# Kernel optimization log

Measured on AMD Instinct MI355X. Metric: run time of the kernel, lower is better.

Reference implementation:

```python
import jax, jax.numpy as jnp
import numpy as np

D, P = 50, 2          # feature dim and max polynomial order (module defaults)
N = 32768             # batch size

def _indexset(d, p):
    # faithful numpy port of indexset(): all multi-indices of total order exactly p
    if d == 1:
        return np.full((1, 1), p, dtype=np.int64)
    blocks = []
    for i in range(p + 1):
        sub = _indexset(d - 1, p - i)
        blocks.append(np.concatenate([np.full((sub.shape[0], 1), i, np.int64), sub], axis=1))
    return np.concatenate(blocks, axis=0)

def _normal_basis(p):
    # faithful numpy port of NormalBasis(): (physicists') Hermite recurrence coefficients
    B = np.zeros((p + 1, p + 1), np.float32)
    B[0, 0] = 1.0
    if p >= 1:
        B[1, 1] = 2.0
    for i in range(1, p):
        B[i + 1, 1:i + 2] = 2.0 * B[i, :i + 1]
        B[i + 1, :i] -= 2.0 * i * B[i - 1, :i]
    return B

def setup_inputs() -> dict:
    key = jax.random.key(0)
    k1, k2 = jax.random.split(key)
    x = jax.random.normal(k1, (N, D), dtype=jnp.float32)
    mean = jax.random.normal(k2, (D,), dtype=jnp.float32)
    var = jnp.ones((D,), dtype=jnp.float32)  # divisor; ones keeps values well-scaled
    oneDbasis = jnp.asarray(_normal_basis(P))                                   # (P+1, P+1)
    idxset = jnp.asarray(np.concatenate([_indexset(D, i) for i in range(P + 1)], axis=0))  # (1326, 50)
    return {"x": x, "mean": mean, "var": var, "oneDbasis": oneDbasis, "idxset": idxset}

def reference(x, mean, var, oneDbasis, idxset):
    p1 = oneDbasis.shape[0]  # p + 1
    # per-dim normalization (original mutates x in place; same math)
    xn = (x - mean) / var                                        # (n, d)
    # PolyVal: powers 0..p then weighted sum over basis coefficients
    x_pows = xn[..., None] ** jnp.arange(p1, dtype=xn.dtype)     # (n, d, p+1)
    polyval = jnp.einsum('ndi,pi->ndp', x_pows, oneDbasis)       # (n, d, p+1)
    n = x.shape[0]
    nbasis = idxset.shape[0]
    # Phi *= polyval[:, j, idxset[:, j]] accumulated over the d feature dims
    def body(Phi, xs):
        pv_j, idx_j = xs                 # pv_j: (n, p+1), idx_j: (nbasis,)
        return Phi * pv_j[:, idx_j], None
    Phi, _ = jax.lax.scan(body,
                          jnp.ones((n, nbasis), dtype=x.dtype),
                          (jnp.transpose(polyval, (1, 0, 2)), idxset.T))
    return Phi
```

## Files before the change

### kernel.cpp

```cpp
#include <hip/hip_runtime.h>
#include <math.h>


#define DD     50
#define P1     3
#define NBASIS 1326
#define NPAIR  (NBASIS / 2)
#define BN     16
#define BLOCK  256

__device__ __forceinline__ int col_desc(int c) {
    if (c == 0) return 0;
    if (c <= DD) return (DD - c) * P1 + 1;
    int t = c - (DD + 1);
    int m = (int)((sqrtf((float)(8 * t + 1)) - 1.0f) * 0.5f);
    while ((m + 1) * (m + 2) / 2 <= t) ++m;
    while (m * (m + 1) / 2 > t) --m;
    int r = t - m * (m + 1) / 2;
    int a = DD - 1 - m;
    if (r == m) return a * P1 + 2;
    return (a * P1 + 1) | (((DD - 1 - r) * P1 + 1) << 8);
}

__global__ __launch_bounds__(BLOCK) void pce_kernel(
    const float* __restrict__ x, const float* __restrict__ mean,
    const float* __restrict__ var, const float* __restrict__ basis,
    float* __restrict__ out, int n)
{
    __shared__ float s_pv[BN][DD * P1 + 2];
    const int tid  = threadIdx.x;
    const int row0 = blockIdx.x * BN;

    float b00 = basis[0], b01 = basis[1], b02 = basis[2];
    float b10 = basis[3], b11 = basis[4], b12 = basis[5];
    float b20 = basis[6], b21 = basis[7], b22 = basis[8];

    const int p0 = tid, p1 = tid + BLOCK, p2 = tid + 2 * BLOCK;
    const bool has2 = (p2 < NPAIR);
    int2 dA = make_int2(col_desc(2 * p0), col_desc(2 * p0 + 1));
    int2 dB = make_int2(col_desc(2 * p1), col_desc(2 * p1 + 1));
    int2 dC = has2 ? make_int2(col_desc(2 * p2), col_desc(2 * p2 + 1))
                   : make_int2(0, 0);

    for (int i = tid; i < BN * DD; i += BLOCK) {
        int r = i / DD, c = i - r * DD;
        float xv = (x[(size_t)(row0 + r) * DD + c] - mean[c]) / var[c];
        float x2 = xv * xv;
        s_pv[r][c * P1 + 0] = b00 + b01 * xv + b02 * x2;
        s_pv[r][c * P1 + 1] = b10 + b11 * xv + b12 * x2;
        s_pv[r][c * P1 + 2] = b20 + b21 * xv + b22 * x2;
    }
    __syncthreads();

    #pragma unroll
    for (int r = 0; r < BN; ++r) {
        const float* pvr = s_pv[r];
        float2* orow = (float2*)(out + (size_t)(row0 + r) * NBASIS);
        float2 v;
        v.x = pvr[dA.x & 0xff] * pvr[dA.x >> 8];
        v.y = pvr[dA.y & 0xff] * pvr[dA.y >> 8];
        orow[p0] = v;
        v.x = pvr[dB.x & 0xff] * pvr[dB.x >> 8];
        v.y = pvr[dB.y & 0xff] * pvr[dB.y >> 8];
        orow[p1] = v;
        if (has2) {
            v.x = pvr[dC.x & 0xff] * pvr[dC.x >> 8];
            v.y = pvr[dC.y & 0xff] * pvr[dC.y >> 8];
            orow[p2] = v;
        }
    }
}

extern "C" void kernel_launch(void* const* d_in, const int* in_sizes, int n_in,
                              void* d_out, int out_size, void* d_ws, size_t ws_size,
                              hipStream_t stream) {
    const float* x     = (const float*)d_in[0];
    const float* mean  = (const float*)d_in[1];
    const float* var   = (const float*)d_in[2];
    const float* basis = (const float*)d_in[3];
    float* out = (float*)d_out;

    const int d = in_sizes[1];
    const int n = in_sizes[0] / d;

    (void)d_ws; (void)ws_size;

    pce_kernel<<<(n + BN - 1) / BN, BLOCK, 0, stream>>>(x, mean, var, basis, out, n);
}
```

Baseline: 184.3 us.

## Restructure basis-product write into 4-wide units with reversed, padded shared table

```diff
diff --git a/kernel.cpp b/kernel.cpp
--- a/kernel.cpp
+++ b/kernel.cpp
@@ -3,70 +3,102 @@
 
 
 #define DD     50
-#define P1     3
 #define NBASIS 1326
-#define NPAIR  (NBASIS / 2)
 #define BN     16
 #define BLOCK  256
-
-__device__ __forceinline__ int col_desc(int c) {
-    if (c == 0) return 0;
-    if (c <= DD) return (DD - c) * P1 + 1;
-    int t = c - (DD + 1);
-    int m = (int)((sqrtf((float)(8 * t + 1)) - 1.0f) * 0.5f);
-    while ((m + 1) * (m + 2) / 2 <= t) ++m;
-    while (m * (m + 1) / 2 > t) --m;
-    int r = t - m * (m + 1) / 2;
-    int a = DD - 1 - m;
-    if (r == m) return a * P1 + 2;
-    return (a * P1 + 1) | (((DD - 1 - r) * P1 + 1) << 8);
-}
+#define RS     104
+#define ONEOFF 52
+#define H2OFF  54
+#define NUNITS 352
 
 __global__ __launch_bounds__(BLOCK) void pce_kernel(
     const float* __restrict__ x, const float* __restrict__ mean,
     const float* __restrict__ var, const float* __restrict__ basis,
     float* __restrict__ out, int n)
 {
-    __shared__ float s_pv[BN][DD * P1 + 2];
+    __shared__ __align__(16) float T[BN][RS];
     const int tid  = threadIdx.x;
     const int row0 = blockIdx.x * BN;
 
-    float b00 = basis[0], b01 = basis[1], b02 = basis[2];
     float b10 = basis[3], b11 = basis[4], b12 = basis[5];
     float b20 = basis[6], b21 = basis[7], b22 = basis[8];
 
-    const int p0 = tid, p1 = tid + BLOCK, p2 = tid + 2 * BLOCK;
-    const bool has2 = (p2 < NPAIR);
-    int2 dA = make_int2(col_desc(2 * p0), col_desc(2 * p0 + 1));
-    int2 dB = make_int2(col_desc(2 * p1), col_desc(2 * p1 + 1));
-    int2 dC = has2 ? make_int2(col_desc(2 * p2), col_desc(2 * p2 + 1))
-                   : make_int2(0, 0);
+    int cols0[2], e0[2], f0off[2], hoff[2], hq[2], nval[2];
+    #pragma unroll
+    for (int s = 0; s < 2; ++s) {
+        int u = tid + s * BLOCK;
+        int C0 = 0, E0 = ONEOFF, F0 = ONEOFF, HO = ONEOFF, HQ = -1, NV = 1;
+        if (u < 12) {
+            C0 = 1 + 4 * u; E0 = 4 * u; NV = 4;
+        } else if (u == 12) {
+            C0 = 49; E0 = 48; NV = 2;
+        } else if (u == 13) {
+            C0 = 0; E0 = ONEOFF; NV = 1;
+        } else if (u < NUNITS) {
+            int u2 = u - 14;
+            int m = (int)((sqrtf((float)(2 * u2) + 1.0f) - 1.0f) * 0.5f);
+            while (2 * (m + 1) * (m + 2) <= u2) ++m;
+            while (m > 0 && 2 * m * (m + 1) > u2) --m;
+            int rem  = u2 - 2 * m * (m + 1);
+            int qoff = rem / (m + 1);
+            int j    = rem - qoff * (m + 1);
+            int q    = 4 * m + qoff;
+            C0 = 51 + (q * (q + 1)) / 2 + 4 * j;
+            E0 = 4 * j;
+            F0 = q;
+            HO = H2OFF + q;
+            HQ = q - 4 * j; if (HQ > 3) HQ = -1;
+            NV = q + 1 - 4 * j; if (NV > 4) NV = 4;
+        }
+        cols0[s] = C0; e0[s] = E0; f0off[s] = F0;
+        hoff[s] = HO; hq[s] = HQ; nval[s] = NV;
+    }
+    const bool has2 = (tid < NUNITS - BLOCK);
 
     for (int i = tid; i < BN * DD; i += BLOCK) {
         int r = i / DD, c = i - r * DD;
         float xv = (x[(size_t)(row0 + r) * DD + c] - mean[c]) / var[c];
         float x2 = xv * xv;
-        s_pv[r][c * P1 + 0] = b00 + b01 * xv + b02 * x2;
-        s_pv[r][c * P1 + 1] = b10 + b11 * xv + b12 * x2;
-        s_pv[r][c * P1 + 2] = b20 + b21 * xv + b22 * x2;
+        int k = (DD - 1) - c;
+        T[r][k]         = b10 + b11 * xv + b12 * x2;
+        T[r][H2OFF + k] = b20 + b21 * xv + b22 * x2;
+    }
+    if (tid < BN) {
+        T[tid][50] = 0.0f; T[tid][51] = 0.0f;
+        T[tid][ONEOFF] = 1.0f; T[tid][53] = 0.0f;
     }
     __syncthreads();
 
     #pragma unroll
     for (int r = 0; r < BN; ++r) {
-        const float* pvr = s_pv[r];
-        float2* orow = (float2*)(out + (size_t)(row0 + r) * NBASIS);
-        float2 v;
-        v.x = pvr[dA.x & 0xff] * pvr[dA.x >> 8];
-        v.y = pvr[dA.y & 0xff] * pvr[dA.y >> 8];
-        orow[p0] = v;
-        v.x = pvr[dB.x & 0xff] * pvr[dB.x >> 8];
-        v.y = pvr[dB.y & 0xff] * pvr[dB.y >> 8];
-        orow[p1] = v;
+        float* o = out + (size_t)(row0 + r) * NBASIS;
+        {
+            float4 v  = *(const float4*)&T[r][e0[0]];
+            float  f0 = T[r][f0off[0]];
+            float  h  = T[r][hoff[0]];
+            float w0 = (hq[0] == 0) ? h : f0 * v.x;
+            float w1 = (hq[0] == 1) ? h : f0 * v.y;
+            float w2 = (hq[0] == 2) ? h : f0 * v.z;
+            float w3 = (hq[0] == 3) ? h : f0 * v.w;
+            float* p = o + cols0[0];
+            p[0] = w0;
+            if (nval[0] > 1) p[1] = w1;
+            if (nval[0] > 2) p[2] = w2;
+            if (nval[0] > 3) p[3] = w3;
+        }
         if (has2) {
-            v.x = pvr[dC.x & 0xff] * pvr[dC.x >> 8];
-            v.y = pvr[dC.y & 0xff] * pvr[dC.y >> 8];
-            orow[p2] = v;
+            float4 v  = *(const float4*)&T[r][e0[1]];
+            float  f0 = T[r][f0off[1]];
+            float  h  = T[r][hoff[1]];
+            float w0 = (hq[1] == 0) ? h : f0 * v.x;
+            float w1 = (hq[1] == 1) ? h : f0 * v.y;
+            float w2 = (hq[1] == 2) ? h : f0 * v.z;
+            float w3 = (hq[1] == 3) ? h : f0 * v.w;
+            float* p = o + cols0[1];
+            p[0] = w0;
+            if (nval[1] > 1) p[1] = w1;
+            if (nval[1] > 2) p[2] = w2;
+            if (nval[1] > 3) p[3] = w3;
         }
     }
 }
```

Result: slower. 210.8 us (+14.4%).
